# Optimization experiments

Hardware: AMD Instinct MI355X
Metric: run time of the kernel (lower is better)

Reference implementation:

```python
import jax, jax.numpy as jnp
import numpy as np


def _conv(x, w, b=None, stride=1, pad=0, dil=1):
    out = jax.lax.conv_general_dilated(
        x, w, (stride, stride), [(pad, pad), (pad, pad)],
        rhs_dilation=(dil, dil),
        dimension_numbers=('NCHW', 'OIHW', 'NCHW'))
    return out if b is None else out + b[None, :, None, None]


def _sobel_base(out_ch, in_ch, k=3):
    # Exactly mirrors SobelConv2d weight construction (4 directional kernels).
    w = np.zeros((out_ch, in_ch, k, k), np.float32)
    m = k // 2
    for idx in range(out_ch):
        if idx % 4 == 0:
            w[idx, :, 0, :] = -1; w[idx, :, 0, m] = -2
            w[idx, :, -1, :] = 1; w[idx, :, -1, m] = 2
        elif idx % 4 == 1:
            w[idx, :, :, 0] = -1; w[idx, :, m, 0] = -2
            w[idx, :, :, -1] = 1; w[idx, :, m, -1] = 2
        elif idx % 4 == 2:
            w[idx, :, 0, 0] = -2
            for i in range(m + 1):
                w[idx, :, m - i, i] = -1
                w[idx, :, k - 1 - i, m + i] = 1
            w[idx, :, -1, -1] = 2
        else:
            w[idx, :, -1, 0] = -2
            for i in range(m + 1):
                w[idx, :, m + i, i] = -1
                w[idx, :, i, m + i] = 1
            w[idx, :, 0, -1] = 2
    return w


def setup_inputs() -> dict:
    key = jax.random.key(0)
    ks = iter(jax.random.split(key, 40))
    def p(shape, s=0.05):
        return jax.random.normal(next(ks), shape, dtype=jnp.float32) * s
    C = 32  # out_ch == sobel_ch
    f32 = jnp.float32
    return dict(
        x=jax.random.normal(next(ks), (8, 1, 256, 256), dtype=f32),
        sobel_base=jnp.asarray(_sobel_base(C, 1)),
        sobel_factor=jnp.ones((C, 1, 1, 1), f32),
        sobel_bias=jnp.zeros((C,), f32),
        f4_w=p((C, C + 1, 3, 3)), f4_b=jnp.zeros((C,), f32),
        ec1_w=p((C, C, 3, 3)), ec1_b=jnp.zeros((C,), f32),
        ec2_w=p((C, C, 3, 3)), ec2_b=jnp.zeros((C,), f32),
        ec3_w=p((C, C, 3, 3)), ec3_b=jnp.zeros((C,), f32),
        gate_w=p((3, 3 * C, 1, 1)), gate_b=jnp.zeros((3,), f32),
        ca1_w=p((C // 16, C, 1, 1)),  # ChannelAttention fc1 (ratio=16), no bias
        ca2_w=p((C, C // 16, 1, 1)),  # fc2, no bias
        sa_w=p((1, 2, 7, 7)),         # SpatialAttention conv, no bias
        p1_w=p((C, C, 1, 1)), p1_b=jnp.zeros((C,), f32),
        f1_w=p((C, C, 3, 3)), f1_b=jnp.zeros((C,), f32),
        p2_w=p((C, 2 * C, 1, 1)), p2_b=jnp.zeros((C,), f32),
        f2_w=p((C, C, 3, 3)), f2_b=jnp.zeros((C,), f32),
        p3_w=p((C, 2 * C, 1, 1)), p3_b=jnp.zeros((C,), f32),
        f3_w=p((C, C, 3, 3)), f3_b=jnp.zeros((C,), f32),
    )


def reference(x, sobel_base, sobel_factor, sobel_bias, f4_w, f4_b,
              ec1_w, ec1_b, ec2_w, ec2_b, ec3_w, ec3_b, gate_w, gate_b,
              ca1_w, ca2_w, sa_w,
              p1_w, p1_b, f1_w, f1_b, p2_w, p2_b, f2_w, f2_b,
              p3_w, p3_b, f3_w, f3_b):
    lrelu = lambda t: jax.nn.leaky_relu(t, 0.01)
    relu = jax.nn.relu
    # Sobel edge extraction (fixed directional kernels scaled by learned factor)
    out0 = _conv(x, sobel_base * sobel_factor, sobel_bias, pad=1)     # [B,32,H,W]
    out1 = jnp.concatenate([x, out0], axis=1)                          # [B,33,H,W]
    out1 = lrelu(_conv(out1, f4_w, f4_b, pad=1))                       # [B,32,H,W]
    # AdaptiveEdgeConnector: multi-dilation convs + softmax gating
    ex = relu(_conv(out1, ec1_w, ec1_b, pad=1))
    ey = relu(_conv(out1, ec2_w, ec2_b, pad=2, dil=2))
    ez = relu(_conv(out1, ec3_w, ec3_b, pad=3, dil=3))
    gates = jax.nn.softmax(_conv(jnp.concatenate([ex, ey, ez], axis=1), gate_w, gate_b), axis=1)
    enh = gates[:, 0:1] * ex + gates[:, 1:2] * ey + gates[:, 2:3] * ez
    # CBAM: channel attention
    avg = jnp.mean(enh, axis=(2, 3), keepdims=True)
    mx = jnp.max(enh, axis=(2, 3), keepdims=True)
    ca = jax.nn.sigmoid(_conv(relu(_conv(avg, ca1_w)), ca2_w)
                        + _conv(relu(_conv(mx, ca1_w)), ca2_w))
    f = ca * enh
    # CBAM: spatial attention
    sa_in = jnp.concatenate([jnp.mean(f, axis=1, keepdims=True),
                             jnp.max(f, axis=1, keepdims=True)], axis=1)
    sa = jax.nn.sigmoid(_conv(sa_in, sa_w, pad=3))
    edge = sa * f
    # Residual merge + cascaded dense conv stages
    out0 = lrelu(out1 + edge)
    t = lrelu(_conv(out0, p1_w, p1_b))
    t = lrelu(_conv(t, f1_w, f1_b, pad=1))
    o1 = jnp.concatenate([out0, t], axis=1)                            # [B,64,H,W]
    t = lrelu(_conv(o1, p2_w, p2_b))
    t = lrelu(_conv(t, f2_w, f2_b, pad=1))
    o2 = jnp.concatenate([out0, t], axis=1)
    t = lrelu(_conv(o2, p3_w, p3_b))
    t = lrelu(_conv(t, f3_w, f3_b, pad=1))
    return jnp.concatenate([out0, t], axis=1)                          # [B,64,H,W]
```

## Files before the change

kernel.cpp:

```cpp
#include <hip/hip_runtime.h>
#include <math.h>

typedef unsigned short u16;
typedef short short8 __attribute__((ext_vector_type(8)));
typedef float f32x4 __attribute__((ext_vector_type(4)));
typedef unsigned short ushort4v __attribute__((ext_vector_type(4)));

#define Hh 256
#define Ww 256
#define Bb 8
#define PW 262
#define PAD 3
#define HPW (Hh * PW)

__device__ __forceinline__ float bf2f(u16 v) {
    unsigned u = ((unsigned)v) << 16;
    union { unsigned u; float f; } c; c.u = u; return c.f;
}
__device__ __forceinline__ u16 f2bf(float f) {
    union { float f; unsigned u; } c; c.f = f;
    unsigned lsb = (c.u >> 16) & 1u;
    c.u += 0x7fffu + lsb;
    return (u16)(c.u >> 16);
}
__device__ __forceinline__ float sigm(float v) { return 1.f / (1.f + expf(-v)); }

template<int ACT, bool F32OUT>
__global__ __launch_bounds__(256) void convs_k(
    const u16* __restrict__ in, const u16* __restrict__ apack,
    const float* __restrict__ bias, void* __restrict__ outp)
{
    __shared__ u16 rows[3][4352];
    const int tid = threadIdx.x, lane = tid & 63, wv = tid >> 6;
    const int b = blockIdx.x & 7;
    const int rest = blockIdx.x >> 3;
    const int h = rest >> 1, half = rest & 1;
    const int pl = wv * 32 + (lane & 15);
    const int icg = lane >> 4;

    for (int idx = tid; idx < 3 * 536; idx += 256) {
        int rr = idx / 536, q = idx % 536;
        int r = h - 1 + rr;
        short8 v = (short8){0, 0, 0, 0, 0, 0, 0, 0};
        if ((unsigned)r < 256u)
            v = *(const short8*)(in + ((size_t)b * HPW + (size_t)r * PW + PAD + half * 128 - 3) * 32
                                 + (size_t)q * 8);
        *(short8*)(&rows[rr][q * 8]) = v;
    }
    __syncthreads();

    f32x4 acc[2][2];
    #pragma unroll
    for (int mf = 0; mf < 2; ++mf)
        #pragma unroll
        for (int nf = 0; nf < 2; ++nf)
            acc[mf][nf] = (f32x4){0.f, 0.f, 0.f, 0.f};

    #pragma unroll
    for (int tap = 0; tap < 9; ++tap) {
        const int kh = tap / 3 - 1, kw = tap % 3 - 1;
        const int ri = 1 + kh;
        short8 a0 = *(const short8*)(apack + ((size_t)(tap * 2 + 0) * 64 + lane) * 8);
        short8 a1 = *(const short8*)(apack + ((size_t)(tap * 2 + 1) * 64 + lane) * 8);
        #pragma unroll
        for (int nf = 0; nf < 2; ++nf) {
            short8 bf = *(const short8*)(&rows[ri][(pl + nf * 16 + kw + 3) * 32 + icg * 8]);
            acc[0][nf] = __builtin_amdgcn_mfma_f32_16x16x32_bf16(a0, bf, acc[0][nf], 0, 0, 0);
            acc[1][nf] = __builtin_amdgcn_mfma_f32_16x16x32_bf16(a1, bf, acc[1][nf], 0, 0, 0);
        }
    }
    const int nl = half * 128 + pl;
    f32x4 bi[2];
    bi[0] = *(const f32x4*)(bias + icg * 4);
    bi[1] = *(const f32x4*)(bias + 16 + icg * 4);
    if (F32OUT) {
        float* dp = (float*)outp + ((size_t)b * 64 + 32) * 65536 + (size_t)h * 256;
        #pragma unroll
        for (int mf = 0; mf < 2; ++mf) {
            const int cob = mf * 16 + icg * 4;
            #pragma unroll
            for (int nf = 0; nf < 2; ++nf) {
                const int w = nl + nf * 16;
                #pragma unroll
                for (int i = 0; i < 4; ++i) {
                    float v = acc[mf][nf][i] + bi[mf][i];
                    if (ACT == 1) v = fmaxf(v, 0.f);
                    if (ACT == 2) v = (v > 0.f) ? v : 0.01f * v;
                    dp[(size_t)(cob + i) * 65536 + w] = v;
                }
            }
        }
    } else {
        const size_t orow = ((size_t)b * HPW + (size_t)h * PW + PAD) * 32;
        u16* out = (u16*)outp;
        #pragma unroll
        for (int mf = 0; mf < 2; ++mf) {
            const int cob = mf * 16 + icg * 4;
            #pragma unroll
            for (int nf = 0; nf < 2; ++nf) {
                ushort4v o;
                #pragma unroll
                for (int i = 0; i < 4; ++i) {
                    float v = acc[mf][nf][i] + bi[mf][i];
                    if (ACT == 1) v = fmaxf(v, 0.f);
                    if (ACT == 2) v = (v > 0.f) ? v : 0.01f * v;
                    o[i] = f2bf(v);
                }
                *(ushort4v*)(out + orow + (size_t)(nl + nf * 16) * 32 + cob) = o;
            }
        }
    }
}

__global__ __launch_bounds__(256) void ecfuse_k(
    const u16* __restrict__ in, const u16* __restrict__ apack,
    const float* __restrict__ b1, const float* __restrict__ b2,
    const float* __restrict__ b3, const float* __restrict__ gw_,
    const float* __restrict__ gb_, u16* __restrict__ enh)
{
    __shared__ u16 rows[3][4352];
    __shared__ float gw[288];
    __shared__ float gb[3];
    __shared__ float bs[96];
    int tid = threadIdx.x;
    for (int i = tid; i < 288; i += 256) gw[i] = gw_[i];
    if (tid < 3) gb[tid] = gb_[tid];
    if (tid < 32) bs[tid] = b1[tid];
    else if (tid < 64) bs[tid] = b2[tid - 32];
    else if (tid < 96) bs[tid] = b3[tid - 64];

    const int lane = tid & 63, wv = tid >> 6;
    const int b = blockIdx.x & 7;
    const int rest = blockIdx.x >> 3;
    const int h = rest >> 1, half = rest & 1;
    const int pl = wv * 32 + (lane & 15);
    const int icg = lane >> 4;

    f32x4 acc[3][2][2];
    #pragma unroll
    for (int cv = 0; cv < 3; ++cv)
        #pragma unroll
        for (int mf = 0; mf < 2; ++mf)
            #pragma unroll
            for (int nf = 0; nf < 2; ++nf)
                acc[cv][mf][nf] = (f32x4){0.f, 0.f, 0.f, 0.f};

    #pragma unroll
    for (int cv = 0; cv < 3; ++cv) {
        const int dil = cv + 1;
        __syncthreads();
        for (int idx = tid; idx < 3 * 536; idx += 256) {
            int rr = idx / 536, q = idx % 536;
            int r = h + (rr - 1) * dil;
            short8 v = (short8){0, 0, 0, 0, 0, 0, 0, 0};
            if ((unsigned)r < 256u)
                v = *(const short8*)(in + ((size_t)b * HPW + (size_t)r * PW + PAD + half * 128 - 3) * 32
                                     + (size_t)q * 8);
            *(short8*)(&rows[rr][q * 8]) = v;
        }
        __syncthreads();
        const u16* ap = apack + (size_t)(cv * 9 * 2) * 512;
        #pragma unroll
        for (int tap = 0; tap < 9; ++tap) {
            const int kh = tap / 3 - 1, kw = tap % 3 - 1;
            const int ri = 1 + kh;
            short8 a0 = *(const short8*)(ap + (size_t)(tap * 2 + 0) * 512 + lane * 8);
            short8 a1 = *(const short8*)(ap + (size_t)(tap * 2 + 1) * 512 + lane * 8);
            #pragma unroll
            for (int nf = 0; nf < 2; ++nf) {
                short8 bf = *(const short8*)(&rows[ri][(pl + nf * 16 + kw * dil + 3) * 32 + icg * 8]);
                acc[cv][0][nf] = __builtin_amdgcn_mfma_f32_16x16x32_bf16(a0, bf, acc[cv][0][nf], 0, 0, 0);
                acc[cv][1][nf] = __builtin_amdgcn_mfma_f32_16x16x32_bf16(a1, bf, acc[cv][1][nf], 0, 0, 0);
            }
        }
    }
    const int nl = half * 128 + pl;
    const size_t orow = ((size_t)b * HPW + (size_t)h * PW + PAD) * 32;
    #pragma unroll
    for (int nf = 0; nf < 2; ++nf) {
        float e[3][2][4];
        float g0 = 0.f, g1 = 0.f, g2 = 0.f;
        #pragma unroll
        for (int cv = 0; cv < 3; ++cv)
            #pragma unroll
            for (int mf = 0; mf < 2; ++mf) {
                const int cob = mf * 16 + icg * 4;
                #pragma unroll
                for (int i = 0; i < 4; ++i) {
                    float v = fmaxf(acc[cv][mf][nf][i] + bs[cv * 32 + cob + i], 0.f);
                    e[cv][mf][i] = v;
                    const int c = cv * 32 + cob + i;
                    g0 = fmaf(gw[c], v, g0);
                    g1 = fmaf(gw[96 + c], v, g1);
                    g2 = fmaf(gw[192 + c], v, g2);
                }
            }
        g0 += __shfl_xor(g0, 16); g0 += __shfl_xor(g0, 32);
        g1 += __shfl_xor(g1, 16); g1 += __shfl_xor(g1, 32);
        g2 += __shfl_xor(g2, 16); g2 += __shfl_xor(g2, 32);
        g0 += gb[0]; g1 += gb[1]; g2 += gb[2];
        float m = fmaxf(g0, fmaxf(g1, g2));
        float e0 = expf(g0 - m), e1 = expf(g1 - m), e2 = expf(g2 - m);
        float inv = 1.f / (e0 + e1 + e2);
        e0 *= inv; e1 *= inv; e2 *= inv;
        #pragma unroll
        for (int mf = 0; mf < 2; ++mf) {
            const int cob = mf * 16 + icg * 4;
            ushort4v o;
            #pragma unroll
            for (int i = 0; i < 4; ++i)
                o[i] = f2bf(e0 * e[0][mf][i] + e1 * e[1][mf][i] + e2 * e[2][mf][i]);
            *(ushort4v*)(enh + orow + (size_t)(nl + nf * 16) * 32 + cob) = o;
        }
    }
}

template<int ICB, int ACT, bool TWO>
__global__ __launch_bounds__(256) void convm_k(
    const u16* __restrict__ in0, const u16* __restrict__ in1,
    const u16* __restrict__ apack, const float* __restrict__ bias,
    u16* __restrict__ out)
{
    constexpr int CS = TWO ? 32 : ICB * 32;
    const int tid = threadIdx.x, lane = tid & 63, wv = tid >> 6;
    const int b = blockIdx.x & 7, h = blockIdx.x >> 3;
    const int nl = (wv << 6) + (lane & 15);
    const int icg = lane >> 4;

    f32x4 acc[2][4];
    #pragma unroll
    for (int mf = 0; mf < 2; ++mf)
        #pragma unroll
        for (int nf = 0; nf < 4; ++nf)
            acc[mf][nf] = (f32x4){0.f, 0.f, 0.f, 0.f};

    #pragma unroll
    for (int s = 0; s < ICB; ++s) {
        short8 a0 = *(const short8*)(apack + ((size_t)(s * 2 + 0) * 64 + lane) * 8);
        short8 a1 = *(const short8*)(apack + ((size_t)(s * 2 + 1) * 64 + lane) * 8);
        const u16* src = TWO ? (s ? in1 : in0) : in0;
        const int icoff = TWO ? 0 : s * 32;
        size_t base = ((size_t)b * HPW + (size_t)h * PW + PAD + nl) * CS + icoff + icg * 8;
        #pragma unroll
        for (int nf = 0; nf < 4; ++nf) {
            short8 bf = *(const short8*)(src + base + (size_t)nf * 16 * CS);
            acc[0][nf] = __builtin_amdgcn_mfma_f32_16x16x32_bf16(a0, bf, acc[0][nf], 0, 0, 0);
            acc[1][nf] = __builtin_amdgcn_mfma_f32_16x16x32_bf16(a1, bf, acc[1][nf], 0, 0, 0);
        }
    }
    const size_t orow = ((size_t)b * HPW + (size_t)h * PW + PAD) * 32;
    #pragma unroll
    for (int mf = 0; mf < 2; ++mf) {
        const int cob = mf * 16 + icg * 4;
        f32x4 bi = *(const f32x4*)(bias + cob);
        #pragma unroll
        for (int nf = 0; nf < 4; ++nf) {
            ushort4v o;
            #pragma unroll
            for (int i = 0; i < 4; ++i) {
                float v = acc[mf][nf][i] + bi[i];
                if (ACT == 1) v = fmaxf(v, 0.f);
                if (ACT == 2) v = (v > 0.f) ? v : 0.01f * v;
                o[i] = f2bf(v);
            }
            *(ushort4v*)(out + orow + (size_t)(nl + nf * 16) * 32 + cob) = o;
        }
    }
}

__global__ void prepack_k(
    const float* __restrict__ f4w, const float* __restrict__ e1w,
    const float* __restrict__ e2w, const float* __restrict__ e3w,
    const float* __restrict__ f1w, const float* __restrict__ f2w,
    const float* __restrict__ f3w, const float* __restrict__ p1w,
    const float* __restrict__ p2w, const float* __restrict__ p3w,
    u16* __restrict__ apack)
{
    int gid = blockIdx.x * 256 + threadIdx.x;
    if (gid >= 77 * 1024) return;
    const int offs[11] = {0, 18, 27, 36, 45, 54, 63, 72, 73, 75, 77};
    int step = gid >> 10, r = gid & 1023;
    int layer = 0;
    while (step >= offs[layer + 1]) layer++;
    int s = step - offs[layer];
    int mf = r >> 9, l = (r >> 3) & 63, j = r & 7;
    int co = mf * 16 + (l & 15);
    int ICB = (layer == 0 || layer == 8 || layer == 9) ? 2 : 1;
    int tap = s / ICB, icb = s % ICB;
    int icl = icb * 32 + (l >> 4) * 8 + j;
    float v = 0.f;
    if (layer == 0)      { if (icl < 33) v = f4w[(co * 33 + icl) * 9 + tap]; }
    else if (layer == 1) v = e1w[(co * 32 + icl) * 9 + tap];
    else if (layer == 2) v = e2w[(co * 32 + icl) * 9 + tap];
    else if (layer == 3) v = e3w[(co * 32 + icl) * 9 + tap];
    else if (layer == 4) v = f1w[(co * 32 + icl) * 9 + tap];
    else if (layer == 5) v = f2w[(co * 32 + icl) * 9 + tap];
    else if (layer == 6) v = f3w[(co * 32 + icl) * 9 + tap];
    else if (layer == 7) v = p1w[co * 32 + icl];
    else if (layer == 8) v = p2w[co * 64 + icl];
    else                 v = p3w[co * 64 + icl];
    apack[gid] = f2bf(v);
}

__global__ __launch_bounds__(256) void prep5_k(
    const float* __restrict__ f4w, const float* __restrict__ f4b,
    const float* __restrict__ sbase, const float* __restrict__ sfac,
    const float* __restrict__ sbias,
    float* __restrict__ w5, float* __restrict__ be)
{
    __shared__ float sF[32 * 33 * 9];
    __shared__ float sS[288];
    __shared__ float sBias[32];
    int t = threadIdx.x;
    for (int i = t; i < 32 * 33 * 9; i += 256) sF[i] = f4w[i];
    for (int i = t; i < 288; i += 256) sS[i] = sbase[i] * sfac[i / 9];
    if (t < 32) sBias[t] = sbias[t];
    __syncthreads();

    for (int idx = t; idx < 800; idx += 256) {
        int co = idx / 25, tap = idx % 25, kh = tap / 5, kw = tap % 5;
        float s = 0.f;
        if (kh >= 1 && kh <= 3 && kw >= 1 && kw <= 3)
            s = sF[(co * 33 + 0) * 9 + (kh - 1) * 3 + (kw - 1)];
        for (int sc = 0; sc < 32; ++sc) {
            #pragma unroll
            for (int a = 0; a < 3; ++a)
                #pragma unroll
                for (int bq = 0; bq < 3; ++bq) {
                    int p = kh - a, q = kw - bq;
                    if (p >= 0 && p < 3 && q >= 0 && q < 3)
                        s = fmaf(sF[(co * 33 + 1 + sc) * 9 + a * 3 + bq],
                                 sS[sc * 9 + p * 3 + q], s);
                }
        }
        w5[idx] = s;
    }
    for (int co = t; co < 32; co += 256) {
        float s = f4b[co];
        for (int sc = 0; sc < 32; ++sc) {
            float wsum = 0.f;
            #pragma unroll
            for (int k = 0; k < 9; ++k) wsum += sF[(co * 33 + 1 + sc) * 9 + k];
            s = fmaf(sBias[sc], wsum, s);
        }
        be[co] = s;
    }
}

__global__ __launch_bounds__(256) void conv5_k(
    const float* __restrict__ x, const float* __restrict__ w5,
    const float* __restrict__ be, u16* __restrict__ out1)
{
    __shared__ float sw[800];
    __shared__ float sb[32];
    int tid = threadIdx.x;
    for (int i = tid; i < 800; i += 256) sw[i] = w5[i];
    if (tid < 32) sb[tid] = be[tid];
    __syncthreads();
    int b = blockIdx.x & 7, h = blockIdx.x >> 3, w = tid;
    const float* xp = x + (size_t)b * 65536;
    float xv[25];
    #pragma unroll
    for (int i = 0; i < 5; ++i) {
        int r = h + i - 2;
        #pragma unroll
        for (int j = 0; j < 5; ++j) {
            int c = w + j - 2;
            xv[i * 5 + j] = ((unsigned)r < 256u && (unsigned)c < 256u)
                            ? xp[r * 256 + c] : 0.f;
        }
    }
    u16* dst = out1 + ((size_t)b * HPW + (size_t)h * PW + PAD + w) * 32;
    #pragma unroll
    for (int cb = 0; cb < 4; ++cb) {
        short8 o;
        #pragma unroll
        for (int j = 0; j < 8; ++j) {
            int co = cb * 8 + j;
            float s = sb[co];
            #pragma unroll
            for (int t2 = 0; t2 < 25; ++t2) s = fmaf(sw[co * 25 + t2], xv[t2], s);
            s = (s > 0.f) ? s : 0.01f * s;
            o[j] = (short)f2bf(s);
        }
        *(short8*)(dst + cb * 8) = o;
    }
    if (tid < 24) {
        int col6 = tid >> 2, chunk = tid & 3;
        int col = (col6 < 3) ? col6 : (256 + PAD + col6 - 3);
        u16* pz = out1 + ((size_t)b * HPW + (size_t)h * PW + col) * 32 + chunk * 8;
        *(short8*)pz = (short8){0, 0, 0, 0, 0, 0, 0, 0};
    }
}

__global__ __launch_bounds__(256) void ringfix_k(
    const float* __restrict__ x, const float* __restrict__ f4w,
    const float* __restrict__ f4b, const float* __restrict__ sbase,
    const float* __restrict__ sfac, const float* __restrict__ sbias,
    u16* __restrict__ out1)
{
    __shared__ float sW[288];
    __shared__ float sB[32];
    __shared__ float sF[32 * 33 * 9];
    __shared__ float sO[66][2][32];
    int tid = threadIdx.x;
    for (int i = tid; i < 288; i += 256) sW[i] = sbase[i] * sfac[i / 9];
    if (tid < 32) sB[tid] = sbias[tid];
    for (int i = tid; i < 32 * 33 * 9; i += 256) sF[i] = f4w[i];
    __syncthreads();

    int blk = blockIdx.x;
    int b = blk & 7, rest = blk >> 3;
    int e = rest >> 2, seg = rest & 3;
    const float* xp = x + (size_t)b * 65536;

    for (int i = tid; i < 66 * 2 * 32; i += 256) {
        int sc = i & 31, rr2 = i >> 5;
        int d = rr2 & 1, ul = rr2 >> 1;
        int ug = seg * 64 - 1 + ul;
        float v = 0.f;
        if ((unsigned)ug < 256u) {
            int h, w;
            if (e == 0)      { h = d;        w = ug; }
            else if (e == 1) { h = 255 - d;  w = ug; }
            else if (e == 2) { h = ug;       w = d; }
            else             { h = ug;       w = 255 - d; }
            float s = sB[sc];
            for (int p = 0; p < 3; ++p)
                for (int q = 0; q < 3; ++q) {
                    int rr = h + p - 1, cc = w + q - 1;
                    if ((unsigned)rr < 256u && (unsigned)cc < 256u)
                        s = fmaf(sW[sc * 9 + p * 3 + q], xp[rr * 256 + cc], s);
                }
            v = s;
        }
        sO[ul][d][sc] = v;
    }
    __syncthreads();

    int pi = tid & 63, cog = tid >> 6;
    int up = seg * 64 + pi;
    int h, w;
    if (e == 0)      { h = 0;   w = up; }
    else if (e == 1) { h = 255; w = up; }
    else if (e == 2) { h = up;  w = 0; }
    else             { h = up;  w = 255; }
    short8 ov;
    for (int cj = 0; cj < 8; ++cj) {
        int co = cog * 8 + cj;
        float acc = f4b[co];
        for (int a = 0; a < 3; ++a)
            for (int bb = 0; bb < 3; ++bb) {
                int hh = h + a - 1, ww = w + bb - 1;
                if ((unsigned)hh < 256u && (unsigned)ww < 256u)
                    acc = fmaf(sF[(co * 33) * 9 + a * 3 + bb], xp[hh * 256 + ww], acc);
                int d, ug;
                if (e == 0)      { d = hh;        ug = ww; }
                else if (e == 1) { d = 255 - hh;  ug = ww; }
                else if (e == 2) { d = ww;        ug = hh; }
                else             { d = 255 - ww;  ug = hh; }
                if (d >= 0 && d < 2 && (unsigned)ug < 256u) {
                    int ul = ug - (seg * 64 - 1);
                    for (int sc = 0; sc < 32; ++sc)
                        acc = fmaf(sF[(co * 33 + 1 + sc) * 9 + a * 3 + bb], sO[ul][d][sc], acc);
                }
            }
        acc = (acc > 0.f) ? acc : 0.01f * acc;
        ov[cj] = (short)f2bf(acc);
    }
    u16* dst = out1 + ((size_t)b * HPW + (size_t)h * PW + PAD + w) * 32 + cog * 8;
    *(short8*)dst = ov;
}

__global__ __launch_bounds__(256) void ca_part_k(
    const u16* __restrict__ enh, float* __restrict__ part)
{
    int blk = blockIdx.x, b = blk & 7, sl = blk >> 3;
    int tid = threadIdx.x, lane = tid & 63, wv = tid >> 6;
    float s[32], m[32];
    #pragma unroll
    for (int c = 0; c < 32; ++c) { s[c] = 0.f; m[c] = -1e30f; }
    for (int k = 0; k < 8; ++k) {
        int px = sl * 2048 + k * 256 + tid;
        int h = px >> 8, w = px & 255;
        size_t off = ((size_t)b * HPW + (size_t)h * PW + PAD + w) * 32;
        #pragma unroll
        for (int cb = 0; cb < 4; ++cb) {
            short8 v = *(const short8*)(enh + off + cb * 8);
            #pragma unroll
            for (int j = 0; j < 8; ++j) {
                float f = bf2f((u16)v[j]);
                s[cb * 8 + j] += f;
                m[cb * 8 + j] = fmaxf(m[cb * 8 + j], f);
            }
        }
    }
    #pragma unroll
    for (int c = 0; c < 32; ++c)
        #pragma unroll
        for (int o = 32; o; o >>= 1) {
            s[c] += __shfl_down(s[c], o);
            m[c] = fmaxf(m[c], __shfl_down(m[c], o));
        }
    __shared__ float ls[4][32], lm[4][32];
    if (lane == 0)
        for (int c = 0; c < 32; ++c) { ls[wv][c] = s[c]; lm[wv][c] = m[c]; }
    __syncthreads();
    if (tid < 32) {
        float ts = 0.f, tm = -1e30f;
        for (int w2 = 0; w2 < 4; ++w2) { ts += ls[w2][tid]; tm = fmaxf(tm, lm[w2][tid]); }
        int bs = b * 32 + sl;
        part[(size_t)(bs * 2 + 0) * 32 + tid] = ts;
        part[(size_t)(bs * 2 + 1) * 32 + tid] = tm;
    }
}

__global__ void ca_final_k(const float* __restrict__ part,
                           const float* __restrict__ w1, const float* __restrict__ w2,
                           float* __restrict__ ca)
{
    int t = threadIdx.x, b = t >> 5, c = t & 31;
    float s = 0.f, m = -1e30f;
    for (int sl = 0; sl < 32; ++sl) {
        int bs = b * 32 + sl;
        s += part[(size_t)(bs * 2 + 0) * 32 + c];
        m = fmaxf(m, part[(size_t)(bs * 2 + 1) * 32 + c]);
    }
    __shared__ float av[8][32], mx[8][32];
    av[b][c] = s * (1.f / 65536.f);
    mx[b][c] = m;
    __syncthreads();
    float sa0 = 0.f, sm0 = 0.f, sa1 = 0.f, sm1 = 0.f;
    for (int k = 0; k < 32; ++k) {
        float wa = w1[k], wb = w1[32 + k];
        sa0 = fmaf(wa, av[b][k], sa0); sm0 = fmaf(wa, mx[b][k], sm0);
        sa1 = fmaf(wb, av[b][k], sa1); sm1 = fmaf(wb, mx[b][k], sm1);
    }
    float h0 = fmaxf(sa0, 0.f) + fmaxf(sm0, 0.f);
    float h1 = fmaxf(sa1, 0.f) + fmaxf(sm1, 0.f);
    ca[t] = sigm(w2[c * 2 + 0] * h0 + w2[c * 2 + 1] * h1);
}

__global__ __launch_bounds__(256) void samap_k(
    const u16* __restrict__ enh, const float* __restrict__ ca,
    float* __restrict__ smap)
{
    __shared__ float sca[256];
    int tid = threadIdx.x;
    sca[tid] = ca[tid];
    __syncthreads();
    int b = blockIdx.x & 7;
    int r = (blockIdx.x >> 3) * 256 + tid;
    if (r >= 262 * 262) return;
    int ph = r / 262, pw = r % 262;
    float mean = 0.f, mxv = 0.f;
    if (ph >= 3 && ph < 259 && pw >= 3 && pw < 259) {
        int h = ph - 3, w = pw - 3;
        size_t off = ((size_t)b * HPW + (size_t)h * PW + PAD + w) * 32;
        float s = 0.f, m = -1e30f;
        #pragma unroll
        for (int cb = 0; cb < 4; ++cb) {
            short8 v = *(const short8*)(enh + off + cb * 8);
            #pragma unroll
            for (int j = 0; j < 8; ++j) {
                float f = bf2f((u16)v[j]) * sca[b * 32 + cb * 8 + j];
                s += f; m = fmaxf(m, f);
            }
        }
        mean = s * (1.f / 32.f); mxv = m;
    }
    smap[((size_t)b * 262 * 262 + (size_t)ph * 262 + pw) * 2 + 0] = mean;
    smap[((size_t)b * 262 * 262 + (size_t)ph * 262 + pw) * 2 + 1] = mxv;
}

__global__ __launch_bounds__(256) void merge_k(
    const float* __restrict__ smap, const float* __restrict__ saw,
    const float* __restrict__ ca, const u16* __restrict__ out1,
    const u16* __restrict__ enh, u16* __restrict__ o0,
    float* __restrict__ dout)
{
    __shared__ float sw[98];
    __shared__ float sca[256];
    int tid = threadIdx.x;
    for (int i = tid; i < 98; i += 256) sw[i] = saw[i];
    sca[tid] = ca[tid];
    __syncthreads();
    int b = blockIdx.x & 7;
    int hw = (blockIdx.x >> 3) * 256 + tid;
    int h = hw >> 8, w = hw & 255;
    const float* sp = smap + (size_t)b * 262 * 262 * 2;
    float acc = 0.f;
    #pragma unroll
    for (int kh = 0; kh < 7; ++kh)
        #pragma unroll
        for (int kw = 0; kw < 7; ++kw) {
            const float* q = sp + ((size_t)(h + kh) * 262 + (w + kw)) * 2;
            acc = fmaf(q[0], sw[kh * 7 + kw], acc);
            acc = fmaf(q[1], sw[49 + kh * 7 + kw], acc);
        }
    float sa = sigm(acc);
    size_t off = ((size_t)b * HPW + (size_t)h * PW + PAD + w) * 32;
    float* dp = dout + (size_t)b * 64 * 65536 + hw;
    #pragma unroll
    for (int cb = 0; cb < 4; ++cb) {
        short8 ve = *(const short8*)(enh + off + cb * 8);
        short8 vo = *(const short8*)(out1 + off + cb * 8);
        short8 o;
        #pragma unroll
        for (int j = 0; j < 8; ++j) {
            float f = sca[b * 32 + cb * 8 + j] * bf2f((u16)ve[j]);
            float v = bf2f((u16)vo[j]) + sa * f;
            v = (v > 0.f) ? v : 0.01f * v;
            o[j] = (short)f2bf(v);
            dp[(size_t)(cb * 8 + j) * 65536] = v;
        }
        *(short8*)(o0 + off + cb * 8) = o;
    }
}

extern "C" void kernel_launch(void* const* d_in, const int* in_sizes, int n_in,
                              void* d_out, int out_size, void* d_ws, size_t ws_size,
                              hipStream_t stream)
{
    (void)in_sizes; (void)n_in; (void)out_size; (void)ws_size;
    const float* x        = (const float*)d_in[0];
    const float* sob_base = (const float*)d_in[1];
    const float* sob_fac  = (const float*)d_in[2];
    const float* sob_bias = (const float*)d_in[3];
    const float* f4_w = (const float*)d_in[4];   const float* f4_b = (const float*)d_in[5];
    const float* ec1_w = (const float*)d_in[6];  const float* ec1_b = (const float*)d_in[7];
    const float* ec2_w = (const float*)d_in[8];  const float* ec2_b = (const float*)d_in[9];
    const float* ec3_w = (const float*)d_in[10]; const float* ec3_b = (const float*)d_in[11];
    const float* gate_w = (const float*)d_in[12]; const float* gate_b = (const float*)d_in[13];
    const float* ca1_w = (const float*)d_in[14]; const float* ca2_w = (const float*)d_in[15];
    const float* sa_w  = (const float*)d_in[16];
    const float* p1_w = (const float*)d_in[17]; const float* p1_b = (const float*)d_in[18];
    const float* f1_w = (const float*)d_in[19]; const float* f1_b = (const float*)d_in[20];
    const float* p2_w = (const float*)d_in[21]; const float* p2_b = (const float*)d_in[22];
    const float* f2_w = (const float*)d_in[23]; const float* f2_b = (const float*)d_in[24];
    const float* p3_w = (const float*)d_in[25]; const float* p3_b = (const float*)d_in[26];
    const float* f3_w = (const float*)d_in[27]; const float* f3_b = (const float*)d_in[28];

    const size_t PB32 = (size_t)Bb * HPW * 32 * 2;
    char* ws = (char*)d_ws;
    u16* Q    = (u16*)(ws);
    u16* O0   = (u16*)(ws + PB32);
    u16* T    = (u16*)(ws + 2 * PB32);
    u16* ENH  = (u16*)(ws + 3 * PB32);
    u16* AP   = (u16*)(ws + 4 * PB32);
    float* W5   = (float*)(ws + 4 * PB32 + 77 * 1024 * 2);
    float* BE   = W5 + 800;
    float* PART = BE + 32;
    float* CA   = PART + 8 * 32 * 2 * 32;

    char* doutc = (char*)d_out;
    float* SMAP = (float*)(doutc + (134217728 - (size_t)Bb * 262 * 262 * 2 * 4));
    float* dout = (float*)d_out;

    dim3 blk(256);

    prepack_k<<<308, blk, 0, stream>>>(f4_w, ec1_w, ec2_w, ec3_w, f1_w, f2_w, f3_w,
                                       p1_w, p2_w, p3_w, AP);
    prep5_k<<<1, blk, 0, stream>>>(f4_w, f4_b, sob_base, sob_fac, sob_bias, W5, BE);
    conv5_k<<<2048, blk, 0, stream>>>(x, W5, BE, Q);
    ringfix_k<<<128, blk, 0, stream>>>(x, f4_w, f4_b, sob_base, sob_fac, sob_bias, Q);
    ecfuse_k<<<4096, blk, 0, stream>>>(Q, AP + 18 * 1024, ec1_b, ec2_b, ec3_b,
                                       gate_w, gate_b, ENH);
    ca_part_k<<<256, blk, 0, stream>>>(ENH, PART);
    ca_final_k<<<1, blk, 0, stream>>>(PART, ca1_w, ca2_w, CA);
    samap_k<<<2152, blk, 0, stream>>>(ENH, CA, SMAP);
    merge_k<<<2048, blk, 0, stream>>>(SMAP, sa_w, CA, Q, ENH, O0, dout);
    convm_k<1, 2, false><<<2048, blk, 0, stream>>>(O0, nullptr, AP + 72 * 1024, p1_b, Q);
    convs_k<2, false><<<4096, blk, 0, stream>>>(Q, AP + 45 * 1024, f1_b, T);
    convm_k<2, 2, true ><<<2048, blk, 0, stream>>>(O0, T, AP + 73 * 1024, p2_b, Q);
    convs_k<2, false><<<4096, blk, 0, stream>>>(Q, AP + 54 * 1024, f2_b, T);
    convm_k<2, 2, true ><<<2048, blk, 0, stream>>>(O0, T, AP + 75 * 1024, p3_b, Q);
    convs_k<2, true ><<<4096, blk, 0, stream>>>(Q, AP + 63 * 1024, f3_b, dout);
}
```

Baseline: 436.5 us.

## Fuse the 1x1 pointwise convs into the merge and 3x3 conv kernels

The p1 1x1 conv is folded into merge_k: the merged row is staged in shared memory and multiplied with MFMA before write-out. The p2 and p3 1x1 convs, which take the concatenation of out0 and the 3x3 output, are folded into the epilogue of the preceding 3x3 conv kernel. That epilogue reuses the shared row buffer as a tile and reads out0 directly from global memory. This removes three separate convm_k launches and the global write and re-read of the intermediate T and Q tensors, at the cost of extra barriers and more work and registers per block.

```diff
diff --git a/kernel.cpp b/kernel.cpp
--- a/kernel.cpp
+++ b/kernel.cpp
@@ -25,10 +25,12 @@
 }
 __device__ __forceinline__ float sigm(float v) { return 1.f / (1.f + expf(-v)); }
 
-template<int ACT, bool F32OUT>
+template<int ACT, bool F32OUT, bool FUSEP>
 __global__ __launch_bounds__(256) void convs_k(
     const u16* __restrict__ in, const u16* __restrict__ apack,
-    const float* __restrict__ bias, void* __restrict__ outp)
+    const float* __restrict__ bias, void* __restrict__ outp,
+    const u16* __restrict__ o0buf, const u16* __restrict__ pw,
+    const float* __restrict__ pb, u16* __restrict__ pout)
 {
     __shared__ u16 rows[3][4352];
     const int tid = threadIdx.x, lane = tid & 63, wv = tid >> 6;
@@ -73,7 +75,72 @@
     f32x4 bi[2];
     bi[0] = *(const f32x4*)(bias + icg * 4);
     bi[1] = *(const f32x4*)(bias + 16 + icg * 4);
-    if (F32OUT) {
+
+    if (FUSEP) {
+        u16* tile = &rows[0][0];
+        __syncthreads();
+        #pragma unroll
+        for (int mf = 0; mf < 2; ++mf) {
+            const int cob = mf * 16 + icg * 4;
+            #pragma unroll
+            for (int nf = 0; nf < 2; ++nf) {
+                ushort4v o;
+                #pragma unroll
+                for (int i = 0; i < 4; ++i) {
+                    float v = acc[mf][nf][i] + bi[mf][i];
+                    v = (v > 0.f) ? v : 0.01f * v;
+                    o[i] = f2bf(v);
+                }
+                *(ushort4v*)(tile + (pl + nf * 16) * 32 + cob) = o;
+            }
+        }
+        __syncthreads();
+        f32x4 acc2[2][2];
+        #pragma unroll
+        for (int mf = 0; mf < 2; ++mf)
+            #pragma unroll
+            for (int nf = 0; nf < 2; ++nf)
+                acc2[mf][nf] = (f32x4){0.f, 0.f, 0.f, 0.f};
+        #pragma unroll
+        for (int s = 0; s < 2; ++s) {
+            short8 pa0 = *(const short8*)(pw + (size_t)(s * 2 + 0) * 512 + lane * 8);
+            short8 pa1 = *(const short8*)(pw + (size_t)(s * 2 + 1) * 512 + lane * 8);
+            #pragma unroll
+            for (int nf = 0; nf < 2; ++nf) {
+                const int px = pl + nf * 16;
+                short8 bf;
+                if (s == 0)
+                    bf = *(const short8*)(o0buf + ((size_t)b * HPW + (size_t)h * PW + PAD + half * 128 + px) * 32 + icg * 8);
+                else
+                    bf = *(const short8*)(tile + px * 32 + icg * 8);
+                acc2[0][nf] = __builtin_amdgcn_mfma_f32_16x16x32_bf16(pa0, bf, acc2[0][nf], 0, 0, 0);
+                acc2[1][nf] = __builtin_amdgcn_mfma_f32_16x16x32_bf16(pa1, bf, acc2[1][nf], 0, 0, 0);
+            }
+        }
+        const size_t orow = ((size_t)b * HPW + (size_t)h * PW + PAD) * 32;
+        #pragma unroll
+        for (int mf = 0; mf < 2; ++mf) {
+            const int cob = mf * 16 + icg * 4;
+            f32x4 pbi = *(const f32x4*)(pb + cob);
+            #pragma unroll
+            for (int nf = 0; nf < 2; ++nf) {
+                ushort4v o;
+                #pragma unroll
+                for (int i = 0; i < 4; ++i) {
+                    float v = acc2[mf][nf][i] + pbi[i];
+                    v = (v > 0.f) ? v : 0.01f * v;
+                    o[i] = f2bf(v);
+                }
+                *(ushort4v*)(pout + orow + (size_t)(nl + nf * 16) * 32 + cob) = o;
+            }
+        }
+        if (tid < 12) {
+            int col3 = tid >> 2, chunk = tid & 3;
+            int col = half ? (256 + PAD + col3) : col3;
+            u16* pz = pout + ((size_t)b * HPW + (size_t)h * PW + col) * 32 + chunk * 8;
+            *(short8*)pz = (short8){0, 0, 0, 0, 0, 0, 0, 0};
+        }
+    } else if (F32OUT) {
         float* dp = (float*)outp + ((size_t)b * 64 + 32) * 65536 + (size_t)h * 256;
         #pragma unroll
         for (int mf = 0; mf < 2; ++mf) {
@@ -211,59 +278,6 @@
             for (int i = 0; i < 4; ++i)
                 o[i] = f2bf(e0 * e[0][mf][i] + e1 * e[1][mf][i] + e2 * e[2][mf][i]);
             *(ushort4v*)(enh + orow + (size_t)(nl + nf * 16) * 32 + cob) = o;
-        }
-    }
-}
-
-template<int ICB, int ACT, bool TWO>
-__global__ __launch_bounds__(256) void convm_k(
-    const u16* __restrict__ in0, const u16* __restrict__ in1,
-    const u16* __restrict__ apack, const float* __restrict__ bias,
-    u16* __restrict__ out)
-{
-    constexpr int CS = TWO ? 32 : ICB * 32;
-    const int tid = threadIdx.x, lane = tid & 63, wv = tid >> 6;
-    const int b = blockIdx.x & 7, h = blockIdx.x >> 3;
-    const int nl = (wv << 6) + (lane & 15);
-    const int icg = lane >> 4;
-
-    f32x4 acc[2][4];
-    #pragma unroll
-    for (int mf = 0; mf < 2; ++mf)
-        #pragma unroll
-        for (int nf = 0; nf < 4; ++nf)
-            acc[mf][nf] = (f32x4){0.f, 0.f, 0.f, 0.f};
-
-    #pragma unroll
-    for (int s = 0; s < ICB; ++s) {
-        short8 a0 = *(const short8*)(apack + ((size_t)(s * 2 + 0) * 64 + lane) * 8);
-        short8 a1 = *(const short8*)(apack + ((size_t)(s * 2 + 1) * 64 + lane) * 8);
-        const u16* src = TWO ? (s ? in1 : in0) : in0;
-        const int icoff = TWO ? 0 : s * 32;
-        size_t base = ((size_t)b * HPW + (size_t)h * PW + PAD + nl) * CS + icoff + icg * 8;
-        #pragma unroll
-        for (int nf = 0; nf < 4; ++nf) {
-            short8 bf = *(const short8*)(src + base + (size_t)nf * 16 * CS);
-            acc[0][nf] = __builtin_amdgcn_mfma_f32_16x16x32_bf16(a0, bf, acc[0][nf], 0, 0, 0);
-            acc[1][nf] = __builtin_amdgcn_mfma_f32_16x16x32_bf16(a1, bf, acc[1][nf], 0, 0, 0);
-        }
-    }
-    const size_t orow = ((size_t)b * HPW + (size_t)h * PW + PAD) * 32;
-    #pragma unroll
-    for (int mf = 0; mf < 2; ++mf) {
-        const int cob = mf * 16 + icg * 4;
-        f32x4 bi = *(const f32x4*)(bias + cob);
-        #pragma unroll
-        for (int nf = 0; nf < 4; ++nf) {
-            ushort4v o;
-            #pragma unroll
-            for (int i = 0; i < 4; ++i) {
-                float v = acc[mf][nf][i] + bi[i];
-                if (ACT == 1) v = fmaxf(v, 0.f);
-                if (ACT == 2) v = (v > 0.f) ? v : 0.01f * v;
-                o[i] = f2bf(v);
-            }
-            *(ushort4v*)(out + orow + (size_t)(nl + nf * 16) * 32 + cob) = o;
         }
     }
 }
@@ -577,17 +591,20 @@
     const float* __restrict__ smap, const float* __restrict__ saw,
     const float* __restrict__ ca, const u16* __restrict__ out1,
     const u16* __restrict__ enh, u16* __restrict__ o0,
-    float* __restrict__ dout)
+    float* __restrict__ dout,
+    const u16* __restrict__ ap1, const float* __restrict__ p1b,
+    u16* __restrict__ p1out)
 {
     __shared__ float sw[98];
     __shared__ float sca[256];
+    __shared__ u16 tile[256 * 32];
     int tid = threadIdx.x;
     for (int i = tid; i < 98; i += 256) sw[i] = saw[i];
     sca[tid] = ca[tid];
     __syncthreads();
     int b = blockIdx.x & 7;
-    int hw = (blockIdx.x >> 3) * 256 + tid;
-    int h = hw >> 8, w = hw & 255;
+    int h = blockIdx.x >> 3;
+    int w = tid;
     const float* sp = smap + (size_t)b * 262 * 262 * 2;
     float acc = 0.f;
     #pragma unroll
@@ -600,7 +617,7 @@
         }
     float sa = sigm(acc);
     size_t off = ((size_t)b * HPW + (size_t)h * PW + PAD + w) * 32;
-    float* dp = dout + (size_t)b * 64 * 65536 + hw;
+    float* dp = dout + (size_t)b * 64 * 65536 + (size_t)h * 256 + w;
     #pragma unroll
     for (int cb = 0; cb < 4; ++cb) {
         short8 ve = *(const short8*)(enh + off + cb * 8);
@@ -615,6 +632,42 @@
             dp[(size_t)(cb * 8 + j) * 65536] = v;
         }
         *(short8*)(o0 + off + cb * 8) = o;
+        *(short8*)(&tile[w * 32 + cb * 8]) = o;
+    }
+    __syncthreads();
+    const int lane = tid & 63, wv = tid >> 6;
+    const int icg = lane >> 4, l15 = lane & 15;
+    f32x4 acc1[2][4];
+    #pragma unroll
+    for (int mf = 0; mf < 2; ++mf)
+        #pragma unroll
+        for (int nf = 0; nf < 4; ++nf)
+            acc1[mf][nf] = (f32x4){0.f, 0.f, 0.f, 0.f};
+    short8 pa0 = *(const short8*)(ap1 + (size_t)0 * 512 + lane * 8);
+    short8 pa1 = *(const short8*)(ap1 + (size_t)1 * 512 + lane * 8);
+    #pragma unroll
+    for (int nf = 0; nf < 4; ++nf) {
+        short8 bf = *(const short8*)(&tile[(wv * 64 + l15 + nf * 16) * 32 + icg * 8]);
+        acc1[0][nf] = __builtin_amdgcn_mfma_f32_16x16x32_bf16(pa0, bf, acc1[0][nf], 0, 0, 0);
+        acc1[1][nf] = __builtin_amdgcn_mfma_f32_16x16x32_bf16(pa1, bf, acc1[1][nf], 0, 0, 0);
+    }
+    const size_t orow = ((size_t)b * HPW + (size_t)h * PW + PAD) * 32;
+    #pragma unroll
+    for (int mf = 0; mf < 2; ++mf) {
+        const int cob = mf * 16 + icg * 4;
+        f32x4 pbi = *(const f32x4*)(p1b + cob);
+        #pragma unroll
+        for (int nf = 0; nf < 4; ++nf) {
+            const int px = wv * 64 + l15 + nf * 16;
+            ushort4v o;
+            #pragma unroll
+            for (int i = 0; i < 4; ++i) {
+                float v = acc1[mf][nf][i] + pbi[i];
+                v = (v > 0.f) ? v : 0.01f * v;
+                o[i] = f2bf(v);
+            }
+            *(ushort4v*)(p1out + orow + (size_t)px * 32 + cob) = o;
+        }
     }
 }
 
@@ -669,11 +722,12 @@
     ca_part_k<<<256, blk, 0, stream>>>(ENH, PART);
     ca_final_k<<<1, blk, 0, stream>>>(PART, ca1_w, ca2_w, CA);
     samap_k<<<2152, blk, 0, stream>>>(ENH, CA, SMAP);
-    merge_k<<<2048, blk, 0, stream>>>(SMAP, sa_w, CA, Q, ENH, O0, dout);
-    convm_k<1, 2, false><<<2048, blk, 0, stream>>>(O0, nullptr, AP + 72 * 1024, p1_b, Q);
-    convs_k<2, false><<<4096, blk, 0, stream>>>(Q, AP + 45 * 1024, f1_b, T);
-    convm_k<2, 2, true ><<<2048, blk, 0, stream>>>(O0, T, AP + 73 * 1024, p2_b, Q);
-    convs_k<2, false><<<4096, blk, 0, stream>>>(Q, AP + 54 * 1024, f2_b, T);
-    convm_k<2, 2, true ><<<2048, blk, 0, stream>>>(O0, T, AP + 75 * 1024, p3_b, Q);
-    convs_k<2, true ><<<4096, blk, 0, stream>>>(Q, AP + 63 * 1024, f3_b, dout);
-}
+    merge_k<<<2048, blk, 0, stream>>>(SMAP, sa_w, CA, Q, ENH, O0, dout,
+                                      AP + 72 * 1024, p1_b, Q);
+    convs_k<2, false, true ><<<4096, blk, 0, stream>>>(Q, AP + 45 * 1024, f1_b, nullptr,
+                                                       O0, AP + 73 * 1024, p2_b, T);
+    convs_k<2, false, true ><<<4096, blk, 0, stream>>>(T, AP + 54 * 1024, f2_b, nullptr,
+                                                       O0, AP + 75 * 1024, p3_b, Q);
+    convs_k<2, true, false><<<4096, blk, 0, stream>>>(Q, AP + 63 * 1024, f3_b, dout,
+                                                      nullptr, nullptr, nullptr, nullptr);
+}
```

Measured after the change: 405.4 us. -7.1%, faster.
